# Performance work log

Measured on AMD Instinct MI355X. Metric: run time of the kernel, lower is better.

Reference implementation:

```python
import jax, jax.numpy as jnp
import numpy as np

TEMPERATURE = 0.1
TIME_THRESHOLD = 365
NEG = -1e9  # stands in for -inf; exp(NEG - max) == 0 exactly in fp32
EPS = 1e-12  # F.normalize eps


def setup_inputs() -> dict:
    key = jax.random.key(0)
    k1, k2, k3 = jax.random.split(key, 3)
    B, D = 8192, 128
    embeddings = jax.random.normal(k1, (B, D), dtype=jnp.float32)
    survival_times = jax.random.randint(k2, (B,), 0, 3650, dtype=jnp.int32)
    censor = jax.random.randint(k3, (B,), 0, 2, dtype=jnp.int32)
    return {"embeddings": embeddings, "survival_times": survival_times, "censor": censor}


def reference(embeddings, survival_times, censor):
    B = embeddings.shape[0]
    # L2 normalize rows (torch F.normalize semantics)
    norm = jnp.maximum(jnp.linalg.norm(embeddings, axis=1, keepdims=True), EPS)
    z = embeddings / norm
    # pairwise cosine similarity / temperature: [B, B]
    sim = jnp.einsum('ik,jk->ij', z, z) / TEMPERATURE
    diag = jnp.eye(B, dtype=bool)
    sim = jnp.where(diag, NEG, sim)  # mask self-similarity
    # positive mask: |t_i - t_j| < threshold, i != j, row i uncensored
    tdiff = jnp.abs(survival_times[:, None] - survival_times[None, :])
    pos = (tdiff < TIME_THRESHOLD) & (~diag) & (censor[:, None] == 1)
    # per-row masked logsumexp reductions
    denominator = jax.nn.logsumexp(sim, axis=1)                      # [B]
    numerator = jax.nn.logsumexp(jnp.where(pos, sim, NEG), axis=1)   # [B]
    has_pos = jnp.any(pos, axis=1)
    per_row = jnp.where(has_pos, denominator - numerator, 0.0)
    cnt = jnp.sum(has_pos.astype(jnp.float32))
    return jnp.where(cnt > 0, jnp.sum(per_row) / jnp.maximum(cnt, 1.0), 0.0)
```

## Files before the change

kernel.cpp:

```cpp
#include <hip/hip_runtime.h>
#include <cstdint>

#define BDIM 8192
#define DDIM 128
#define JS 32
#define NIU 128

#define ZH_OFF 0
#define ZL_OFF (2 * 1024 * 1024)
#define RL_OFF (4 * 1024 * 1024)
#define CNT_OFF (RL_OFF + BDIM * 4)
#define P_OFF (RL_OFF + 65536)
#define PART_OFF (P_OFF + BDIM * JS * 8)

typedef __attribute__((ext_vector_type(8))) short bf16x8;
typedef __attribute__((ext_vector_type(4))) float f32x4;

__device__ __forceinline__ short f2bf(float f) {
  unsigned u = __float_as_uint(f);
  unsigned r = (u + 0x7fffu + ((u >> 16) & 1u)) >> 16;
  return (short)r;
}
__device__ __forceinline__ float bf2f(short h) {
  return __uint_as_float(((unsigned)(unsigned short)h) << 16);
}


__global__ __launch_bounds__(1024) void ck_compact(
    const int* __restrict__ censor, int* __restrict__ rowlist, int* __restrict__ cnt)
{
  const int t = threadIdx.x;
  const int lane = t & 63, wv = t >> 6;
  int flags[8], loc = 0;
  const int base = t * 8;
#pragma unroll
  for (int u = 0; u < 8; ++u) { flags[u] = (censor[base + u] == 1); loc += flags[u]; }
  int sc = loc;
#pragma unroll
  for (int m = 1; m < 64; m <<= 1) {
    const int v = __shfl_up(sc, m, 64);
    if (lane >= m) sc += v;
  }
  __shared__ int wtot[16], woff[16];
  if (lane == 63) wtot[wv] = sc;
  __syncthreads();
  if (t == 0) {
    int run = 0;
#pragma unroll
    for (int i = 0; i < 16; ++i) { woff[i] = run; run += wtot[i]; }
  }
  __syncthreads();
  int off = woff[wv] + sc - loc;
#pragma unroll
  for (int u = 0; u < 8; ++u)
    if (flags[u]) rowlist[off++] = base + u;
  if (t == 1023) cnt[0] = off;
}

__global__ __launch_bounds__(256) void ck_normalize(
    const float* __restrict__ emb, short* __restrict__ ZhT, short* __restrict__ ZlT)
{
  __shared__ float zl[16][132];
  __shared__ float pr[16][16];
  __shared__ float inv[16];
  const int t = threadIdx.x, R = blockIdx.x;
  const int r16 = t >> 4, seg = t & 15;
  const float4* src = (const float4*)(emb + (size_t)(R * 16 + r16) * DDIM + seg * 8);
  const float4 v0 = src[0], v1 = src[1];
  float* zr = &zl[r16][seg * 8];
  zr[0] = v0.x; zr[1] = v0.y; zr[2] = v0.z; zr[3] = v0.w;
  zr[4] = v1.x; zr[5] = v1.y; zr[6] = v1.z; zr[7] = v1.w;
  pr[r16][seg] = v0.x * v0.x + v0.y * v0.y + v0.z * v0.z + v0.w * v0.w +
                 v1.x * v1.x + v1.y * v1.y + v1.z * v1.z + v1.w * v1.w;
  __syncthreads();
  if (t < 16) {
    float ss = 0.f;
#pragma unroll
    for (int s = 0; s < 16; ++s) ss += pr[t][s];
    inv[t] = 1.0f / fmaxf(sqrtf(ss), 1e-12f);
  }
  __syncthreads();
  const int kc = t >> 6, half = (t >> 4) & 3, r16w = t & 15;
  const float iv = inv[r16w];
  const float* zs = &zl[r16w][(kc * 4 + half) * 8];
  short hs[8], ls[8];
#pragma unroll
  for (int j = 0; j < 8; ++j) {
    const float z = zs[j] * iv;
    const short h = f2bf(z);
    hs[j] = h;
    ls[j] = f2bf(z - bf2f(h));
  }
  const int dst = R * 2048 + t * 8;
  *(bf16x8*)(ZhT + dst) = *(const bf16x8*)hs;
  *(bf16x8*)(ZlT + dst) = *(const bf16x8*)ls;
}

__global__ __launch_bounds__(256) void ck_main(
    const short* __restrict__ ZhT, const short* __restrict__ ZlT,
    const int* __restrict__ rowlist, const int* __restrict__ cntp,
    const int* __restrict__ times, float2* __restrict__ P2)
{
  const int cnt = *cntp;
  const int wid = blockIdx.x * 4 + (threadIdx.x >> 6);
  const int iu = wid >> 5;
  const int js = wid & (JS - 1);
  if (iu * 64 >= cnt) return;
  const int lane = threadIdx.x & 63;
  const int half = lane >> 4;
  const int ll = lane & 15;

  int rbase[4];
#pragma unroll
  for (int a = 0; a < 4; ++a) {
    int c = iu * 64 + a * 16 + ll;
    if (c >= cnt) c = cnt - 1;
    const int r = rowlist[c];
    rbase[a] = (r >> 4) * 2048 + (r & 15) * 8;
  }
  bf16x8 ah[4][4], al[4][4];
#pragma unroll
  for (int a = 0; a < 4; ++a)
#pragma unroll
    for (int kc = 0; kc < 4; ++kc) {
      ah[a][kc] = *(const bf16x8*)(ZhT + rbase[a] + kc * 512 + half * 128);
      al[a][kc] = *(const bf16x8*)(ZlT + rbase[a] + kc * 512 + half * 128);
    }

  int giE[4][4], tiE[4][4];
#pragma unroll
  for (int a = 0; a < 4; ++a)
#pragma unroll
    for (int r = 0; r < 4; ++r) {
      const int idx = iu * 64 + a * 16 + half * 4 + r;
      const bool vi = (idx < cnt);
      const int gi = vi ? rowlist[idx] : -1;
      giE[a][r] = vi ? gi : -1;
      tiE[a][r] = vi ? times[gi] : -1000000;
    }

  float sd[4][4] = {{0.f}}, sn[4][4] = {{0.f}};

  for (int st = 0; st < 4; ++st) {
    const int jb = js * 256 + st * 64;
    const int jR = jb >> 4;
    f32x4 acc[4][4];
#pragma unroll
    for (int a = 0; a < 4; ++a)
#pragma unroll
      for (int b = 0; b < 4; ++b) acc[a][b] = (f32x4){0.f, 0.f, 0.f, 0.f};

#pragma unroll
    for (int kc = 0; kc < 4; ++kc) {
      bf16x8 bh[4], bl[4];
#pragma unroll
      for (int b = 0; b < 4; ++b) {
        const int o = (jR + b) * 2048 + kc * 512 + lane * 8;
        bh[b] = *(const bf16x8*)(ZhT + o);
        bl[b] = *(const bf16x8*)(ZlT + o);
      }
#pragma unroll
      for (int a = 0; a < 4; ++a)
#pragma unroll
        for (int b = 0; b < 4; ++b)
          acc[a][b] = __builtin_amdgcn_mfma_f32_16x16x32_bf16(ah[a][kc], bh[b], acc[a][b], 0, 0, 0);
#pragma unroll
      for (int a = 0; a < 4; ++a)
#pragma unroll
        for (int b = 0; b < 4; ++b)
          acc[a][b] = __builtin_amdgcn_mfma_f32_16x16x32_bf16(ah[a][kc], bl[b], acc[a][b], 0, 0, 0);
#pragma unroll
      for (int a = 0; a < 4; ++a)
#pragma unroll
        for (int b = 0; b < 4; ++b)
          acc[a][b] = __builtin_amdgcn_mfma_f32_16x16x32_bf16(al[a][kc], bh[b], acc[a][b], 0, 0, 0);
    }

    int jg[4], tJ[4];
#pragma unroll
    for (int b = 0; b < 4; ++b) {
      jg[b] = jb + b * 16 + ll;
      tJ[b] = times[jg[b]];
    }
#pragma unroll
    for (int a = 0; a < 4; ++a)
#pragma unroll
      for (int r = 0; r < 4; ++r) {
        const int gi = giE[a][r], ti = tiE[a][r];
        float d = 0.f, n = 0.f;
#pragma unroll
        for (int b = 0; b < 4; ++b) {
          const float s = acc[a][b][r] * 10.0f;
          float pv = __expf(s - 10.0f);
          if (gi == jg[b]) pv = 0.f;
          d += pv;
          int td = ti - tJ[b];
          td = td < 0 ? -td : td;
          if (td < 365) n += pv;
        }
        sd[a][r] += d;
        sn[a][r] += n;
      }
  }

#pragma unroll
  for (int a = 0; a < 4; ++a)
#pragma unroll
    for (int r = 0; r < 4; ++r) {
      float d = sd[a][r], n = sn[a][r];
#pragma unroll
      for (int m = 1; m <= 8; m <<= 1) {
        d += __shfl_xor(d, m, 64);
        n += __shfl_xor(n, m, 64);
      }
      const int idx = iu * 64 + a * 16 + half * 4 + r;
      if (ll == 0 && idx < cnt) P2[idx * JS + js] = make_float2(d, n);
    }
}

__global__ __launch_bounds__(256) void ck_fin_a(
    const float2* __restrict__ P2, const int* __restrict__ cntp,
    float2* __restrict__ part)
{
  const int cnt = *cntp;
  const int t = threadIdx.x;
  const int idx = blockIdx.x * 256 + t;
  float lsum = 0.f, lcnt = 0.f;
  if (idx < cnt) {
    const float4* p = (const float4*)(P2 + (size_t)idx * JS);
    float d = 0.f, n = 0.f;
#pragma unroll
    for (int u = 0; u < 16; ++u) {
      const float4 v = p[u];
      d += v.x + v.z;
      n += v.y + v.w;
    }
    if (n > 0.f) { lsum = logf(d) - logf(n); lcnt = 1.f; }
  }
  __shared__ float s1[256], s2[256];
  s1[t] = lsum; s2[t] = lcnt;
  __syncthreads();
  for (int s = 128; s > 0; s >>= 1) {
    if (t < s) { s1[t] += s1[t + s]; s2[t] += s2[t + s]; }
    __syncthreads();
  }
  if (t == 0) part[blockIdx.x] = make_float2(s1[0], s2[0]);
}

__global__ __launch_bounds__(64) void ck_fin_b(
    const float2* __restrict__ part, float* __restrict__ out)
{
  const int t = threadIdx.x;
  float s = 0.f, c = 0.f;
  if (t < 32) { const float2 v = part[t]; s = v.x; c = v.y; }
#pragma unroll
  for (int m = 1; m < 64; m <<= 1) {
    s += __shfl_xor(s, m, 64);
    c += __shfl_xor(c, m, 64);
  }
  if (t == 0) out[0] = (c > 0.f) ? s / fmaxf(c, 1.f) : 0.f;
}

extern "C" void kernel_launch(void* const* d_in, const int* in_sizes, int n_in,
                              void* d_out, int out_size, void* d_ws, size_t ws_size,
                              hipStream_t stream) {
  const float* emb  = (const float*)d_in[0];
  const int* times  = (const int*)d_in[1];
  const int* censor = (const int*)d_in[2];
  float* out = (float*)d_out;

  char* ws = (char*)d_ws;
  short* ZhT   = (short*)(ws + ZH_OFF);
  short* ZlT   = (short*)(ws + ZL_OFF);
  int* rowlist = (int*)(ws + RL_OFF);
  int* cnt     = (int*)(ws + CNT_OFF);
  float2* P2   = (float2*)(ws + P_OFF);
  float2* part = (float2*)(ws + PART_OFF);

  ck_compact<<<1, 1024, 0, stream>>>(censor, rowlist, cnt);
  ck_normalize<<<BDIM / 16, 256, 0, stream>>>(emb, ZhT, ZlT);
  ck_main<<<NIU * JS / 4, 256, 0, stream>>>(ZhT, ZlT, rowlist, cnt, times, P2);
  ck_fin_a<<<BDIM / 256, 256, 0, stream>>>(P2, cnt, part);
  ck_fin_b<<<1, 64, 0, stream>>>(part, out);
}
```

Measured before the change: 131.3 us.

## Fuse compact into normalize, software-pipeline main loop with smaller tiles

Merges the censor compaction into the normalize kernel as an extra block, which saves one launch. The main kernel now uses 64x32 accumulator tiles instead of 64x64 and no longer keeps the low-part A fragments resident; it reloads them per k-chunk instead. B and A-low loads are double-buffered so they overlap the MFMAs, and launch_bounds(256,2) is set for occupancy. Block mapping now shares js across the 4 waves in a block for B-tile locality, and the time-window test is packed into a single unsigned compare. The trade-off is more reloads of A-low and more frequent epilogues per MFMA, in exchange for fewer registers and latency hiding.

```diff
diff --git a/kernel.cpp b/kernel.cpp
--- a/kernel.cpp
+++ b/kernel.cpp
@@ -4,7 +4,6 @@
 #define BDIM 8192
 #define DDIM 128
 #define JS 32
-#define NIU 128
 
 #define ZH_OFF 0
 #define ZL_OFF (2 * 1024 * 1024)
@@ -26,44 +25,52 @@
 }
 
 
-__global__ __launch_bounds__(1024) void ck_compact(
-    const int* __restrict__ censor, int* __restrict__ rowlist, int* __restrict__ cnt)
-{
-  const int t = threadIdx.x;
-  const int lane = t & 63, wv = t >> 6;
-  int flags[8], loc = 0;
-  const int base = t * 8;
-#pragma unroll
-  for (int u = 0; u < 8; ++u) { flags[u] = (censor[base + u] == 1); loc += flags[u]; }
-  int sc = loc;
-#pragma unroll
-  for (int m = 1; m < 64; m <<= 1) {
-    const int v = __shfl_up(sc, m, 64);
-    if (lane >= m) sc += v;
-  }
-  __shared__ int wtot[16], woff[16];
-  if (lane == 63) wtot[wv] = sc;
-  __syncthreads();
-  if (t == 0) {
-    int run = 0;
-#pragma unroll
-    for (int i = 0; i < 16; ++i) { woff[i] = run; run += wtot[i]; }
-  }
-  __syncthreads();
-  int off = woff[wv] + sc - loc;
-#pragma unroll
-  for (int u = 0; u < 8; ++u)
-    if (flags[u]) rowlist[off++] = base + u;
-  if (t == 1023) cnt[0] = off;
-}
-
-__global__ __launch_bounds__(256) void ck_normalize(
-    const float* __restrict__ emb, short* __restrict__ ZhT, short* __restrict__ ZlT)
+__global__ __launch_bounds__(256) void ck_prep(
+    const float* __restrict__ emb, const int* __restrict__ censor,
+    short* __restrict__ ZhT, short* __restrict__ ZlT,
+    int* __restrict__ rowlist, int* __restrict__ cnt)
 {
   __shared__ float zl[16][132];
   __shared__ float pr[16][16];
   __shared__ float inv[16];
-  const int t = threadIdx.x, R = blockIdx.x;
+  __shared__ int wtot[4], woff[4];
+
+  const int t = threadIdx.x;
+  if (blockIdx.x == 512) {
+    const int lane = t & 63, wv = t >> 6;
+    const int4* c4 = (const int4*)(censor + t * 32);
+    unsigned fm = 0;
+#pragma unroll
+    for (int q = 0; q < 8; ++q) {
+      const int4 v = c4[q];
+      fm |= (unsigned)(v.x == 1) << (q * 4 + 0);
+      fm |= (unsigned)(v.y == 1) << (q * 4 + 1);
+      fm |= (unsigned)(v.z == 1) << (q * 4 + 2);
+      fm |= (unsigned)(v.w == 1) << (q * 4 + 3);
+    }
+    const int loc = __popc(fm);
+    int sc = loc;
+#pragma unroll
+    for (int m = 1; m < 64; m <<= 1) {
+      const int u = __shfl_up(sc, m, 64);
+      if (lane >= m) sc += u;
+    }
+    if (lane == 63) wtot[wv] = sc;
+    __syncthreads();
+    if (t == 0) {
+      int run = 0;
+#pragma unroll
+      for (int i = 0; i < 4; ++i) { woff[i] = run; run += wtot[i]; }
+    }
+    __syncthreads();
+    int off = woff[wv] + sc - loc;
+    for (int u = 0; u < 32; ++u)
+      if ((fm >> u) & 1) rowlist[off++] = t * 32 + u;
+    if (t == 255) cnt[0] = off;
+    return;
+  }
+
+  const int R = blockIdx.x;
   const int r16 = t >> 4, seg = t & 15;
   const float4* src = (const float4*)(emb + (size_t)(R * 16 + r16) * DDIM + seg * 8);
   const float4 v0 = src[0], v1 = src[1];
@@ -96,15 +103,15 @@
   *(bf16x8*)(ZlT + dst) = *(const bf16x8*)ls;
 }
 
-__global__ __launch_bounds__(256) void ck_main(
+__global__ __launch_bounds__(256, 2) void ck_main(
     const short* __restrict__ ZhT, const short* __restrict__ ZlT,
     const int* __restrict__ rowlist, const int* __restrict__ cntp,
     const int* __restrict__ times, float2* __restrict__ P2)
 {
   const int cnt = *cntp;
-  const int wid = blockIdx.x * 4 + (threadIdx.x >> 6);
-  const int iu = wid >> 5;
-  const int js = wid & (JS - 1);
+  const int w = threadIdx.x >> 6;
+  const int js = blockIdx.x & 31;
+  const int iu = (blockIdx.x >> 5) * 4 + w;
   if (iu * 64 >= cnt) return;
   const int lane = threadIdx.x & 63;
   const int half = lane >> 4;
@@ -118,89 +125,102 @@
     const int r = rowlist[c];
     rbase[a] = (r >> 4) * 2048 + (r & 15) * 8;
   }
-  bf16x8 ah[4][4], al[4][4];
+
+  bf16x8 ah[4][4];
 #pragma unroll
   for (int a = 0; a < 4; ++a)
 #pragma unroll
-    for (int kc = 0; kc < 4; ++kc) {
+    for (int kc = 0; kc < 4; ++kc)
       ah[a][kc] = *(const bf16x8*)(ZhT + rbase[a] + kc * 512 + half * 128);
-      al[a][kc] = *(const bf16x8*)(ZlT + rbase[a] + kc * 512 + half * 128);
-    }
-
-  int giE[4][4], tiE[4][4];
+
+  int meta[4][4];
 #pragma unroll
   for (int a = 0; a < 4; ++a)
 #pragma unroll
     for (int r = 0; r < 4; ++r) {
       const int idx = iu * 64 + a * 16 + half * 4 + r;
-      const bool vi = (idx < cnt);
-      const int gi = vi ? rowlist[idx] : -1;
-      giE[a][r] = vi ? gi : -1;
-      tiE[a][r] = vi ? times[gi] : -1000000;
+      const bool vi = idx < cnt;
+      const int gi = rowlist[vi ? idx : 0];
+      const int taP = vi ? (times[gi] + 364) : 50000;
+      meta[a][r] = (taP << 16) | (vi ? gi : 0xFFFF);
     }
 
   float sd[4][4] = {{0.f}}, sn[4][4] = {{0.f}};
-
-  for (int st = 0; st < 4; ++st) {
-    const int jb = js * 256 + st * 64;
-    const int jR = jb >> 4;
-    f32x4 acc[4][4];
+  f32x4 acc[4][2];
+#pragma unroll
+  for (int a = 0; a < 4; ++a)
+#pragma unroll
+    for (int b = 0; b < 2; ++b) acc[a][b] = (f32x4){0.f, 0.f, 0.f, 0.f};
+
+  bf16x8 bh[2][2], bl[2][2], alb[2][4];
+  int tJ[2][2];
+  const int jsT = js * 16;
+
+  auto LP = [&](int p, int par) {
+    const int st = p >> 2, kc = p & 3;
+    const int o = (jsT + st * 2) * 2048 + kc * 512 + lane * 8;
+    bh[par][0] = *(const bf16x8*)(ZhT + o);
+    bh[par][1] = *(const bf16x8*)(ZhT + o + 2048);
+    bl[par][0] = *(const bf16x8*)(ZlT + o);
+    bl[par][1] = *(const bf16x8*)(ZlT + o + 2048);
 #pragma unroll
     for (int a = 0; a < 4; ++a)
-#pragma unroll
-      for (int b = 0; b < 4; ++b) acc[a][b] = (f32x4){0.f, 0.f, 0.f, 0.f};
-
-#pragma unroll
-    for (int kc = 0; kc < 4; ++kc) {
-      bf16x8 bh[4], bl[4];
-#pragma unroll
-      for (int b = 0; b < 4; ++b) {
-        const int o = (jR + b) * 2048 + kc * 512 + lane * 8;
-        bh[b] = *(const bf16x8*)(ZhT + o);
-        bl[b] = *(const bf16x8*)(ZlT + o);
-      }
+      alb[par][a] = *(const bf16x8*)(ZlT + rbase[a] + kc * 512 + half * 128);
+    if (kc == 0) {
+      const int jb = js * 256 + st * 32;
+      tJ[st & 1][0] = times[jb + ll];
+      tJ[st & 1][1] = times[jb + 16 + ll];
+    }
+  };
+
+  LP(0, 0);
+#pragma unroll
+  for (int p = 0; p < 32; ++p) {
+    const int par = p & 1, st = p >> 2, kc = p & 3;
+    if (p + 1 < 32) LP(p + 1, par ^ 1);
+
+#pragma unroll
+    for (int a = 0; a < 4; ++a)
+#pragma unroll
+      for (int b = 0; b < 2; ++b)
+        acc[a][b] = __builtin_amdgcn_mfma_f32_16x16x32_bf16(ah[a][kc], bh[par][b], acc[a][b], 0, 0, 0);
+#pragma unroll
+    for (int a = 0; a < 4; ++a)
+#pragma unroll
+      for (int b = 0; b < 2; ++b)
+        acc[a][b] = __builtin_amdgcn_mfma_f32_16x16x32_bf16(ah[a][kc], bl[par][b], acc[a][b], 0, 0, 0);
+#pragma unroll
+    for (int a = 0; a < 4; ++a)
+#pragma unroll
+      for (int b = 0; b < 2; ++b)
+        acc[a][b] = __builtin_amdgcn_mfma_f32_16x16x32_bf16(alb[par][a], bh[par][b], acc[a][b], 0, 0, 0);
+
+    if (kc == 3) {
+      const int stp = st & 1;
 #pragma unroll
       for (int a = 0; a < 4; ++a)
 #pragma unroll
-        for (int b = 0; b < 4; ++b)
-          acc[a][b] = __builtin_amdgcn_mfma_f32_16x16x32_bf16(ah[a][kc], bh[b], acc[a][b], 0, 0, 0);
+        for (int r = 0; r < 4; ++r) {
+          const int m_ = meta[a][r];
+          const int gi = m_ & 0xFFFF;
+          const unsigned taP = ((unsigned)m_) >> 16;
+          float d = 0.f, n = 0.f;
+#pragma unroll
+          for (int b = 0; b < 2; ++b) {
+            const int jgb = js * 256 + st * 32 + b * 16 + ll;
+            float pv = __expf(fmaf(acc[a][b][r], 10.f, -10.f));
+            pv = (gi == jgb) ? 0.f : pv;
+            d += pv;
+            n += ((unsigned)(taP - (unsigned)tJ[stp][b]) <= 728u) ? pv : 0.f;
+          }
+          sd[a][r] += d;
+          sn[a][r] += n;
+        }
 #pragma unroll
       for (int a = 0; a < 4; ++a)
 #pragma unroll
-        for (int b = 0; b < 4; ++b)
-          acc[a][b] = __builtin_amdgcn_mfma_f32_16x16x32_bf16(ah[a][kc], bl[b], acc[a][b], 0, 0, 0);
-#pragma unroll
-      for (int a = 0; a < 4; ++a)
-#pragma unroll
-        for (int b = 0; b < 4; ++b)
-          acc[a][b] = __builtin_amdgcn_mfma_f32_16x16x32_bf16(al[a][kc], bh[b], acc[a][b], 0, 0, 0);
-    }
-
-    int jg[4], tJ[4];
-#pragma unroll
-    for (int b = 0; b < 4; ++b) {
-      jg[b] = jb + b * 16 + ll;
-      tJ[b] = times[jg[b]];
-    }
-#pragma unroll
-    for (int a = 0; a < 4; ++a)
-#pragma unroll
-      for (int r = 0; r < 4; ++r) {
-        const int gi = giE[a][r], ti = tiE[a][r];
-        float d = 0.f, n = 0.f;
-#pragma unroll
-        for (int b = 0; b < 4; ++b) {
-          const float s = acc[a][b][r] * 10.0f;
-          float pv = __expf(s - 10.0f);
-          if (gi == jg[b]) pv = 0.f;
-          d += pv;
-          int td = ti - tJ[b];
-          td = td < 0 ? -td : td;
-          if (td < 365) n += pv;
-        }
-        sd[a][r] += d;
-        sn[a][r] += n;
-      }
+        for (int b = 0; b < 2; ++b) acc[a][b] = (f32x4){0.f, 0.f, 0.f, 0.f};
+    }
   }
 
 #pragma unroll
@@ -214,7 +234,7 @@
         n += __shfl_xor(n, m, 64);
       }
       const int idx = iu * 64 + a * 16 + half * 4 + r;
-      if (ll == 0 && idx < cnt) P2[idx * JS + js] = make_float2(d, n);
+      if (ll == 0 && idx < cnt) P2[(size_t)idx * JS + js] = make_float2(d, n);
     }
 }
 
@@ -277,9 +297,8 @@
   float2* P2   = (float2*)(ws + P_OFF);
   float2* part = (float2*)(ws + PART_OFF);
 
-  ck_compact<<<1, 1024, 0, stream>>>(censor, rowlist, cnt);
-  ck_normalize<<<BDIM / 16, 256, 0, stream>>>(emb, ZhT, ZlT);
-  ck_main<<<NIU * JS / 4, 256, 0, stream>>>(ZhT, ZlT, rowlist, cnt, times, P2);
-  ck_fin_a<<<BDIM / 256, 256, 0, stream>>>(P2, cnt, part);
+  ck_prep<<<513, 256, 0, stream>>>(emb, censor, ZhT, ZlT, rowlist, cnt);
+  ck_main<<<1024, 256, 0, stream>>>(ZhT, ZlT, rowlist, cnt, times, P2);
+  ck_fin_a<<<32, 256, 0, stream>>>(P2, cnt, part);
   ck_fin_b<<<1, 64, 0, stream>>>(part, out);
 }
```

Result: slower. 257.3 us (+95.9%).
